# Kernel tuning notes

Hardware: AMD Instinct MI355X
Metric: run time of the kernel (lower is better)

## Reference

```python
import jax, jax.numpy as jnp
import numpy as np

C_CLIP = 10.0  # Bello et al. logit clipping constant (init arg C)


def setup_inputs() -> dict:
    key = jax.random.key(0)
    k1, k2, k3, k4, k5 = jax.random.split(key, 5)
    B, S, D = 64, 2048, 512
    scale = 1.0 / np.sqrt(D)  # ~torch Linear default init scale
    src = jax.random.normal(k1, (B, S, D), dtype=jnp.float32)
    tgt = jax.random.normal(k2, (B, 1, D), dtype=jnp.float32)
    W_q = jax.random.normal(k3, (D, D), dtype=jnp.float32) * scale
    W_ref = jax.random.normal(k4, (D, D), dtype=jnp.float32) * scale
    v = jax.random.uniform(k5, (D,), dtype=jnp.float32)  # uniform_(0, 1) as in source
    return {"src": src, "tgt": tgt, "W_q": W_q, "W_ref": W_ref, "v": v}


def reference(src, tgt, W_q, W_ref, v):
    # h = tanh(W_q(tgt) + W_ref(src))  -> [B, S, D] (tgt broadcasts over S)
    h = jnp.tanh(tgt @ W_q.T + src @ W_ref.T)
    # u = bmm(v, h^T) -> [B, 1, S]
    u = jnp.einsum("bsd,d->bs", h, v)[:, None, :]
    # logit clipping: C * tanh(u)
    logit = C_CLIP * jnp.tanh(u)
    probs = jax.nn.softmax(logit, axis=-1)  # [B, 1, S]
    # d_prime = bmm(probs, src) -> [B, 1, D]  ('Sup' path glimpse)
    d_prime = jnp.einsum("bqs,bsd->bqd", probs, src)
    return (d_prime, probs, logit)
```

## Files before the change

kernel.cpp:

```cpp
#include <hip/hip_runtime.h>
#include <math.h>

#define NB 64
#define NS 2048
#define ND 512
#define MTOT (NB * NS)
#define CCLIP 10.0f

typedef _Float16 f16x8 __attribute__((ext_vector_type(8)));
typedef _Float16 f16x4 __attribute__((ext_vector_type(4)));
typedef float f32x4 __attribute__((ext_vector_type(4)));

__device__ __forceinline__ void gl2lds16(const void* g, void* l) {
  __builtin_amdgcn_global_load_lds(
      (const __attribute__((address_space(1))) void*)(uintptr_t)g,
      (__attribute__((address_space(3))) void*)(uintptr_t)l, 16, 0, 0);
}

__device__ __forceinline__ float tanh_fast(float x) {
  float e = __expf(2.f * x);
  return 1.f - 2.f * __builtin_amdgcn_rcpf(e + 1.f);
}

__global__ __launch_bounds__(256) void cvtw_kernel(
    const float4* __restrict__ w4, _Float16* __restrict__ WhA) {
  const int idx = blockIdx.x * 256 + threadIdx.x;
  const int d = idx >> 7;
  const int k = (idx & 127) << 2;
  float4 x = w4[idx];
  f16x4 o;
  o[0] = (_Float16)x.x; o[1] = (_Float16)x.y;
  o[2] = (_Float16)x.z; o[3] = (_Float16)x.w;
  const int kt = k >> 5;
  const int kg = (k >> 3) & 3;
  const int h = k & 7;
  *(f16x4*)(WhA + ((size_t)((kt * 4 + kg) * 512 + d) * 8 + h)) = o;
}

__global__ __launch_bounds__(256) void qk_kernel(const float* __restrict__ tgt,
                                                 const float* __restrict__ Wq,
                                                 float* __restrict__ q_ws) {
  const int b = blockIdx.x >> 1;
  const int d = ((blockIdx.x & 1) << 8) + threadIdx.x;
  __shared__ float tl[ND];
  tl[threadIdx.x] = tgt[b * ND + threadIdx.x];
  tl[threadIdx.x + 256] = tgt[b * ND + threadIdx.x + 256];
  __syncthreads();
  const float4* wr = (const float4*)(Wq + (size_t)d * ND);
  float acc = 0.f;
#pragma unroll 8
  for (int k4 = 0; k4 < ND / 4; ++k4) {
    float4 w4 = wr[k4];
    acc += w4.x * tl[4 * k4 + 0] + w4.y * tl[4 * k4 + 1] +
           w4.z * tl[4 * k4 + 2] + w4.w * tl[4 * k4 + 3];
  }
  q_ws[b * ND + d] = acc;
}

__global__ __launch_bounds__(256, 2) void gemm_kernel(
    const float* __restrict__ src, const _Float16* __restrict__ WhA,
    const float* __restrict__ q_ws, const float* __restrict__ v,
    float* __restrict__ out_logit, float* __restrict__ out_probs_w,
    float* __restrict__ dp_ws) {
  __shared__ __align__(16) _Float16 sA[2][4 * 64 * 8];
  __shared__ __align__(16) _Float16 sB[2][4 * 512 * 8];
  __shared__ float ured[4 * 64];
  __shared__ float wsh[64];

  const int tid = threadIdx.x;
  const int lane = tid & 63;
  const int w = tid >> 6;
  const int s0 = blockIdx.x << 6;
  const int bb = blockIdx.x >> 5;

  const int quad = lane >> 4;
  const int l15 = lane & 15;

  const int ar = tid >> 2;
  const int akg = tid & 3;
  const float4* ap =
      (const float4*)(src + ((size_t)(s0 + ar) << 9)) + akg * 2;
  const int aoff = (akg * 64 + ar) * 8;

  const char* gB = (const char*)WhA;

  f32x4 acc[4][8];
#pragma unroll
  for (int i = 0; i < 4; ++i)
#pragma unroll
    for (int j = 0; j < 8; ++j) acc[i][j] = (f32x4){0.f, 0.f, 0.f, 0.f};

#pragma unroll
  for (int i = 0; i < 8; ++i) {
    const int c = w * 8 + i;
    gl2lds16(gB + c * 1024 + lane * 16, (char*)&sB[0][0] + c * 1024);
  }
  {
    float4 x0 = ap[0];
    float4 x1 = ap[1];
    f16x8 h;
    h[0] = (_Float16)x0.x; h[1] = (_Float16)x0.y;
    h[2] = (_Float16)x0.z; h[3] = (_Float16)x0.w;
    h[4] = (_Float16)x1.x; h[5] = (_Float16)x1.y;
    h[6] = (_Float16)x1.z; h[7] = (_Float16)x1.w;
    *(f16x8*)(&sA[0][0] + aoff) = h;
  }
  __syncthreads();

  int buf = 0;
  for (int kt = 0; kt < 16; ++kt) {
    const int nb = buf ^ 1;
    float4 x0, x1;
    if (kt < 15) {
#pragma unroll
      for (int i = 0; i < 8; ++i) {
        const int c = w * 8 + i;
        gl2lds16(gB + (size_t)(kt + 1) * 32768 + c * 1024 + lane * 16,
                 (char*)&sB[nb][0] + c * 1024);
      }
      x0 = ap[(kt + 1) * 8];
      x1 = ap[(kt + 1) * 8 + 1];
    }
    f16x8 af[4], bf[8];
#pragma unroll
    for (int i = 0; i < 4; ++i)
      af[i] = *(const f16x8*)(&sA[buf][0] + (quad * 64 + 16 * i + l15) * 8);
#pragma unroll
    for (int j = 0; j < 8; ++j)
      bf[j] = *(const f16x8*)(&sB[buf][0] +
                              (quad * 512 + w * 128 + 16 * j + l15) * 8);
#pragma unroll
    for (int i = 0; i < 4; ++i)
#pragma unroll
      for (int j = 0; j < 8; ++j)
        acc[i][j] = __builtin_amdgcn_mfma_f32_16x16x32_f16(af[i], bf[j],
                                                           acc[i][j], 0, 0, 0);
    if (kt < 15) {
      f16x8 h;
      h[0] = (_Float16)x0.x; h[1] = (_Float16)x0.y;
      h[2] = (_Float16)x0.z; h[3] = (_Float16)x0.w;
      h[4] = (_Float16)x1.x; h[5] = (_Float16)x1.y;
      h[6] = (_Float16)x1.z; h[7] = (_Float16)x1.w;
      *(f16x8*)(&sA[nb][0] + aoff) = h;
    }
    __syncthreads();
    buf = nb;
  }

  float pu[4][4];
#pragma unroll
  for (int i = 0; i < 4; ++i)
#pragma unroll
    for (int r = 0; r < 4; ++r) pu[i][r] = 0.f;

#pragma unroll
  for (int j = 0; j < 8; ++j) {
    const int dl = w * 128 + 16 * j + l15;
    const float qq = q_ws[bb * ND + dl];
    const float vv = v[dl];
#pragma unroll
    for (int i = 0; i < 4; ++i) {
      f32x4 a = acc[i][j];
#pragma unroll
      for (int r = 0; r < 4; ++r) pu[i][r] += tanh_fast(a[r] + qq) * vv;
    }
  }

#pragma unroll
  for (int i = 0; i < 4; ++i)
#pragma unroll
    for (int r = 0; r < 4; ++r) {
      float x = pu[i][r];
      x += __shfl_xor(x, 1, 16);
      x += __shfl_xor(x, 2, 16);
      x += __shfl_xor(x, 4, 16);
      x += __shfl_xor(x, 8, 16);
      pu[i][r] = x;
    }

  if (l15 == 0) {
#pragma unroll
    for (int i = 0; i < 4; ++i)
#pragma unroll
      for (int r = 0; r < 4; ++r)
        ured[w * 64 + 16 * i + quad * 4 + r] = pu[i][r];
  }
  __syncthreads();
  if (tid < 64) {
    const float u =
        ured[tid] + ured[64 + tid] + ured[128 + tid] + ured[192 + tid];
    const float lg = CCLIP * tanhf(u);
    out_logit[s0 + tid] = lg;
    const float wexp = expf(lg - CCLIP);
    out_probs_w[s0 + tid] = wexp;
    wsh[tid] = wexp;
  }
  __syncthreads();

  const int c4 = tid & 127;
  const int half = tid >> 7;
  const float4* sp = (const float4*)(src + ((size_t)s0 << 9)) + c4;
  float dx = 0.f, dy = 0.f, dz = 0.f, dw = 0.f;
  const int r0 = half << 5;
#pragma unroll 4
  for (int r = r0; r < r0 + 32; ++r) {
    const float wr = wsh[r];
    const float4 x = sp[(size_t)r * 128];
    dx += wr * x.x; dy += wr * x.y; dz += wr * x.z; dw += wr * x.w;
  }
  float4* red4 = (float4*)&sA[0][0];
  if (half) {
    float4 o; o.x = dx; o.y = dy; o.z = dz; o.w = dw;
    red4[c4] = o;
  }
  __syncthreads();
  if (!half) {
    float4 o = red4[c4];
    o.x += dx; o.y += dy; o.z += dz; o.w += dw;
    *(float4*)(dp_ws + (size_t)blockIdx.x * ND + (c4 << 2)) = o;
  }
}

__global__ __launch_bounds__(256) void fin_kernel(
    const float* __restrict__ dp_ws, float* __restrict__ out_dp,
    float* __restrict__ out_probs) {
  const int b = blockIdx.x;
  const int tid = threadIdx.x;
  __shared__ float red[4];
  __shared__ float s_inv;

  float x = 0.f;
  for (int idx = tid; idx < NS; idx += 256) x += out_probs[b * NS + idx];
#pragma unroll
  for (int m = 32; m; m >>= 1) x += __shfl_xor(x, m, 64);
  if ((tid & 63) == 0) red[tid >> 6] = x;
  __syncthreads();
  if (tid == 0) s_inv = 1.f / (red[0] + red[1] + red[2] + red[3]);
  __syncthreads();
  const float inv = s_inv;

  for (int idx = tid; idx < NS; idx += 256)
    out_probs[b * NS + idx] *= inv;

  for (int d = tid; d < ND; d += 256) {
    float acc = 0.f;
#pragma unroll 8
    for (int ch = 0; ch < 32; ++ch)
      acc += dp_ws[(size_t)(b * 32 + ch) * ND + d];
    out_dp[b * ND + d] = acc * inv;
  }
}

extern "C" void kernel_launch(void* const* d_in, const int* in_sizes, int n_in,
                              void* d_out, int out_size, void* d_ws,
                              size_t ws_size, hipStream_t stream) {
  const float* src = (const float*)d_in[0];
  const float* tgt = (const float*)d_in[1];
  const float* Wq = (const float*)d_in[2];
  const float* Wref = (const float*)d_in[3];
  const float* v = (const float*)d_in[4];

  float* out = (float*)d_out;
  float* out_dp = out;
  float* out_probs = out + NB * ND;
  float* out_logit = out + NB * ND + NB * NS;

  char* ws = (char*)d_ws;
  _Float16* WhA = (_Float16*)ws;
  float* q_ws = (float*)(ws + 524288);
  float* dp_ws = (float*)(ws + 655360);

  cvtw_kernel<<<256, 256, 0, stream>>>((const float4*)Wref, WhA);
  qk_kernel<<<2 * NB, 256, 0, stream>>>(tgt, Wq, q_ws);
  gemm_kernel<<<MTOT / 64, 256, 0, stream>>>(src, WhA, q_ws, v, out_logit,
                                             out_probs, dp_ws);
  fin_kernel<<<NB, 256, 0, stream>>>(dp_ws, out_dp, out_probs);
}
```

Baseline: 447.9 us.

## Use 128-row tiles with 8 waves, triple-buffered weight tiles and swizzled A LDS

The GEMM block doubles to 128 rows of src and 512 threads. Each group of 4 waves shares one fully loaded weight K-tile, which halves how many times the fp16 weights are fetched per row. The weight tile moves to a 3-stage LDS ring with a prefetch distance of two and explicit vmcnt waits in place of __syncthreads. The A tile uses an XOR-swizzled layout to reduce LDS bank conflicts. In exchange it uses more LDS per block (about 112KB), which may limit residency to one block per CU, and the partial-sum reduction for d_prime widens to four parts.

Result: no change. 441.4 us (-1.4%).

```diff
diff --git a/kernel.cpp b/kernel.cpp
--- a/kernel.cpp
+++ b/kernel.cpp
@@ -57,21 +57,23 @@
   q_ws[b * ND + d] = acc;
 }
 
-__global__ __launch_bounds__(256, 2) void gemm_kernel(
+__global__ __launch_bounds__(512, 2) void gemm_kernel(
     const float* __restrict__ src, const _Float16* __restrict__ WhA,
     const float* __restrict__ q_ws, const float* __restrict__ v,
     float* __restrict__ out_logit, float* __restrict__ out_probs_w,
     float* __restrict__ dp_ws) {
-  __shared__ __align__(16) _Float16 sA[2][4 * 64 * 8];
-  __shared__ __align__(16) _Float16 sB[2][4 * 512 * 8];
-  __shared__ float ured[4 * 64];
-  __shared__ float wsh[64];
+  __shared__ __align__(16) _Float16 sBall[3 * 16384];
+  __shared__ __align__(16) _Float16 sAall[2 * 4096];
+  __shared__ float ured[4 * 128];
+  __shared__ float wsh[128];
 
   const int tid = threadIdx.x;
   const int lane = tid & 63;
   const int w = tid >> 6;
-  const int s0 = blockIdx.x << 6;
-  const int bb = blockIdx.x >> 5;
+  const int h = w >> 2;
+  const int cq = w & 3;
+  const int s0 = blockIdx.x << 7;
+  const int bb = blockIdx.x >> 4;
 
   const int quad = lane >> 4;
   const int l15 = lane & 15;
@@ -80,7 +82,7 @@
   const int akg = tid & 3;
   const float4* ap =
       (const float4*)(src + ((size_t)(s0 + ar) << 9)) + akg * 2;
-  const int aoff = (akg * 64 + ar) * 8;
+  const int aoff = akg * 1024 + ((ar ^ (akg << 2)) << 3);
 
   const char* gB = (const char*)WhA;
 
@@ -90,61 +92,86 @@
 #pragma unroll
     for (int j = 0; j < 8; ++j) acc[i][j] = (f32x4){0.f, 0.f, 0.f, 0.f};
 
-#pragma unroll
-  for (int i = 0; i < 8; ++i) {
-    const int c = w * 8 + i;
-    gl2lds16(gB + c * 1024 + lane * 16, (char*)&sB[0][0] + c * 1024);
-  }
+  float4 x0 = ap[0];
+  float4 x1 = ap[1];
   {
-    float4 x0 = ap[0];
-    float4 x1 = ap[1];
-    f16x8 h;
-    h[0] = (_Float16)x0.x; h[1] = (_Float16)x0.y;
-    h[2] = (_Float16)x0.z; h[3] = (_Float16)x0.w;
-    h[4] = (_Float16)x1.x; h[5] = (_Float16)x1.y;
-    h[6] = (_Float16)x1.z; h[7] = (_Float16)x1.w;
-    *(f16x8*)(&sA[0][0] + aoff) = h;
-  }
-  __syncthreads();
-
-  int buf = 0;
+    f16x8 hh;
+    hh[0] = (_Float16)x0.x; hh[1] = (_Float16)x0.y;
+    hh[2] = (_Float16)x0.z; hh[3] = (_Float16)x0.w;
+    hh[4] = (_Float16)x1.x; hh[5] = (_Float16)x1.y;
+    hh[6] = (_Float16)x1.z; hh[7] = (_Float16)x1.w;
+    *(f16x8*)(sAall + aoff) = hh;
+  }
+#pragma unroll
+  for (int i = 0; i < 4; ++i) {
+    const int c = w * 4 + i;
+    gl2lds16(gB + c * 1024 + lane * 16, (char*)sBall + c * 1024);
+  }
+  x0 = ap[8];
+  x1 = ap[9];
+#pragma unroll
+  for (int i = 0; i < 4; ++i) {
+    const int c = w * 4 + i;
+    gl2lds16(gB + 32768 + c * 1024 + lane * 16,
+             (char*)(sBall + 16384) + c * 1024);
+  }
+  __builtin_amdgcn_sched_barrier(0);
+  asm volatile("s_waitcnt vmcnt(0)" ::: "memory");
+  asm volatile("s_waitcnt lgkmcnt(0)" ::: "memory");
+  __builtin_amdgcn_s_barrier();
+  __builtin_amdgcn_sched_barrier(0);
+
   for (int kt = 0; kt < 16; ++kt) {
-    const int nb = buf ^ 1;
-    float4 x0, x1;
+    const _Float16* sB = sBall + (kt % 3) * 16384;
+    const _Float16* sA = sAall + (kt & 1) * 4096;
+
+    f16x8 af[4], bf[8];
+#pragma unroll
+    for (int i = 0; i < 4; ++i) {
+      const int row = h * 64 + 16 * i + l15;
+      af[i] = *(const f16x8*)(sA + quad * 1024 + ((row ^ (quad << 2)) << 3));
+    }
+#pragma unroll
+    for (int j = 0; j < 8; ++j)
+      bf[j] = *(const f16x8*)(sB +
+                              ((quad * 512 + cq * 128 + 16 * j + l15) << 3));
+
     if (kt < 15) {
-#pragma unroll
-      for (int i = 0; i < 8; ++i) {
-        const int c = w * 8 + i;
-        gl2lds16(gB + (size_t)(kt + 1) * 32768 + c * 1024 + lane * 16,
-                 (char*)&sB[nb][0] + c * 1024);
+      f16x8 hh;
+      hh[0] = (_Float16)x0.x; hh[1] = (_Float16)x0.y;
+      hh[2] = (_Float16)x0.z; hh[3] = (_Float16)x0.w;
+      hh[4] = (_Float16)x1.x; hh[5] = (_Float16)x1.y;
+      hh[6] = (_Float16)x1.z; hh[7] = (_Float16)x1.w;
+      *(f16x8*)(sAall + ((kt + 1) & 1) * 4096 + aoff) = hh;
+    }
+    if (kt < 14) {
+      x0 = ap[(kt + 2) * 8];
+      x1 = ap[(kt + 2) * 8 + 1];
+      char* sBn = (char*)(sBall + ((kt + 2) % 3) * 16384);
+#pragma unroll
+      for (int i = 0; i < 4; ++i) {
+        const int c = w * 4 + i;
+        gl2lds16(gB + (size_t)(kt + 2) * 32768 + c * 1024 + lane * 16,
+                 sBn + c * 1024);
       }
-      x0 = ap[(kt + 1) * 8];
-      x1 = ap[(kt + 1) * 8 + 1];
-    }
-    f16x8 af[4], bf[8];
-#pragma unroll
-    for (int i = 0; i < 4; ++i)
-      af[i] = *(const f16x8*)(&sA[buf][0] + (quad * 64 + 16 * i + l15) * 8);
-#pragma unroll
-    for (int j = 0; j < 8; ++j)
-      bf[j] = *(const f16x8*)(&sB[buf][0] +
-                              (quad * 512 + w * 128 + 16 * j + l15) * 8);
+    }
+
 #pragma unroll
     for (int i = 0; i < 4; ++i)
 #pragma unroll
       for (int j = 0; j < 8; ++j)
         acc[i][j] = __builtin_amdgcn_mfma_f32_16x16x32_f16(af[i], bf[j],
                                                            acc[i][j], 0, 0, 0);
-    if (kt < 15) {
-      f16x8 h;
-      h[0] = (_Float16)x0.x; h[1] = (_Float16)x0.y;
-      h[2] = (_Float16)x0.z; h[3] = (_Float16)x0.w;
-      h[4] = (_Float16)x1.x; h[5] = (_Float16)x1.y;
-      h[6] = (_Float16)x1.z; h[7] = (_Float16)x1.w;
-      *(f16x8*)(&sA[nb][0] + aoff) = h;
-    }
-    __syncthreads();
-    buf = nb;
+
+    __builtin_amdgcn_sched_barrier(0);
+    if (kt < 14) {
+      asm volatile("s_waitcnt vmcnt(6)" ::: "memory");
+    } else {
+      asm volatile("s_waitcnt vmcnt(0)" ::: "memory");
+    }
+    asm volatile("s_waitcnt lgkmcnt(0)" ::: "memory");
+    __builtin_amdgcn_s_barrier();
+    __builtin_amdgcn_sched_barrier(0);
   }
 
   float pu[4][4];
@@ -155,7 +182,7 @@
 
 #pragma unroll
   for (int j = 0; j < 8; ++j) {
-    const int dl = w * 128 + 16 * j + l15;
+    const int dl = cq * 128 + 16 * j + l15;
     const float qq = q_ws[bb * ND + dl];
     const float vv = v[dl];
 #pragma unroll
@@ -183,12 +210,12 @@
     for (int i = 0; i < 4; ++i)
 #pragma unroll
       for (int r = 0; r < 4; ++r)
-        ured[w * 64 + 16 * i + quad * 4 + r] = pu[i][r];
-  }
-  __syncthreads();
-  if (tid < 64) {
+        ured[cq * 128 + h * 64 + 16 * i + quad * 4 + r] = pu[i][r];
+  }
+  __syncthreads();
+  if (tid < 128) {
     const float u =
-        ured[tid] + ured[64 + tid] + ured[128 + tid] + ured[192 + tid];
+        ured[tid] + ured[128 + tid] + ured[256 + tid] + ured[384 + tid];
     const float lg = CCLIP * tanhf(u);
     out_logit[s0 + tid] = lg;
     const float wexp = expf(lg - CCLIP);
@@ -198,25 +225,32 @@
   __syncthreads();
 
   const int c4 = tid & 127;
-  const int half = tid >> 7;
+  const int part = tid >> 7;
   const float4* sp = (const float4*)(src + ((size_t)s0 << 9)) + c4;
   float dx = 0.f, dy = 0.f, dz = 0.f, dw = 0.f;
-  const int r0 = half << 5;
+  const int r0 = part << 5;
 #pragma unroll 4
   for (int r = r0; r < r0 + 32; ++r) {
     const float wr = wsh[r];
     const float4 x = sp[(size_t)r * 128];
     dx += wr * x.x; dy += wr * x.y; dz += wr * x.z; dw += wr * x.w;
   }
-  float4* red4 = (float4*)&sA[0][0];
-  if (half) {
+  float4* red4 = (float4*)sBall;
+  {
     float4 o; o.x = dx; o.y = dy; o.z = dz; o.w = dw;
-    red4[c4] = o;
-  }
-  __syncthreads();
-  if (!half) {
-    float4 o = red4[c4];
-    o.x += dx; o.y += dy; o.z += dz; o.w += dw;
+    red4[part * 128 + c4] = o;
+  }
+  __syncthreads();
+  if (tid < 128) {
+    float4 a0 = red4[c4];
+    float4 a1 = red4[128 + c4];
+    float4 a2 = red4[256 + c4];
+    float4 a3 = red4[384 + c4];
+    float4 o;
+    o.x = a0.x + a1.x + a2.x + a3.x;
+    o.y = a0.y + a1.y + a2.y + a3.y;
+    o.z = a0.z + a1.z + a2.z + a3.z;
+    o.w = a0.w + a1.w + a2.w + a3.w;
     *(float4*)(dp_ws + (size_t)blockIdx.x * ND + (c4 << 2)) = o;
   }
 }
@@ -244,9 +278,9 @@
 
   for (int d = tid; d < ND; d += 256) {
     float acc = 0.f;
-#pragma unroll 8
-    for (int ch = 0; ch < 32; ++ch)
-      acc += dp_ws[(size_t)(b * 32 + ch) * ND + d];
+#pragma unroll
+    for (int ch = 0; ch < 16; ++ch)
+      acc += dp_ws[(size_t)(b * 16 + ch) * ND + d];
     out_dp[b * ND + d] = acc * inv;
   }
 }
@@ -272,7 +306,7 @@
 
   cvtw_kernel<<<256, 256, 0, stream>>>((const float4*)Wref, WhA);
   qk_kernel<<<2 * NB, 256, 0, stream>>>(tgt, Wq, q_ws);
-  gemm_kernel<<<MTOT / 64, 256, 0, stream>>>(src, WhA, q_ws, v, out_logit,
-                                             out_probs, dp_ws);
+  gemm_kernel<<<MTOT / 128, 512, 0, stream>>>(src, WhA, q_ws, v, out_logit,
+                                              out_probs, dp_ws);
   fin_kernel<<<NB, 256, 0, stream>>>(dp_ws, out_dp, out_probs);
 }
```

## Load W_ref fragments directly from global into registers instead of LDS staging

Applied to the files above, without the earlier changes.

Converts W_ref into a pre-swizzled fp16 layout in which each lane's MFMA B-fragment is a contiguous 16-byte load, so the GEMM reads B straight from global/L2 into registers. This drops the large sB LDS double buffer and the global-to-LDS copies. It also XOR-swizzles the sA layout to avoid LDS bank conflicts and issues the next A tile's load and store before the MFMAs. The smaller LDS footprint could allow more resident blocks, but every block now re-reads W_ref from cache each k-step with less latency hiding, since the B loads are not prefetched.

Measured after the change: 453.9 us. Within noise of the previous version (+1.3%).

```diff
diff --git a/kernel.cpp b/kernel.cpp
--- a/kernel.cpp
+++ b/kernel.cpp
@@ -11,30 +11,29 @@
 typedef _Float16 f16x4 __attribute__((ext_vector_type(4)));
 typedef float f32x4 __attribute__((ext_vector_type(4)));
 
-__device__ __forceinline__ void gl2lds16(const void* g, void* l) {
-  __builtin_amdgcn_global_load_lds(
-      (const __attribute__((address_space(1))) void*)(uintptr_t)g,
-      (__attribute__((address_space(3))) void*)(uintptr_t)l, 16, 0, 0);
-}
-
 __device__ __forceinline__ float tanh_fast(float x) {
   float e = __expf(2.f * x);
   return 1.f - 2.f * __builtin_amdgcn_rcpf(e + 1.f);
 }
 
-__global__ __launch_bounds__(256) void cvtw_kernel(
-    const float4* __restrict__ w4, _Float16* __restrict__ WhA) {
-  const int idx = blockIdx.x * 256 + threadIdx.x;
-  const int d = idx >> 7;
-  const int k = (idx & 127) << 2;
-  float4 x = w4[idx];
-  f16x4 o;
-  o[0] = (_Float16)x.x; o[1] = (_Float16)x.y;
-  o[2] = (_Float16)x.z; o[3] = (_Float16)x.w;
-  const int kt = k >> 5;
-  const int kg = (k >> 3) & 3;
-  const int h = k & 7;
-  *(f16x4*)(WhA + ((size_t)((kt * 4 + kg) * 512 + d) * 8 + h)) = o;
+__global__ __launch_bounds__(256) void cvtw2_kernel(
+    const float* __restrict__ Wref, _Float16* __restrict__ Wc) {
+  const int g = blockIdx.x * 256 + threadIdx.x;
+  const int lane = g & 63;
+  const int rest = g >> 6;
+  const int c32 = rest & 31;
+  const int kt = rest >> 5;
+  const int col = c32 * 16 + (lane & 15);
+  const int k = kt * 32 + ((lane >> 4) & 3) * 8;
+  const float4* in = (const float4*)(Wref + (size_t)col * ND + k);
+  float4 a = in[0];
+  float4 b = in[1];
+  f16x8 o;
+  o[0] = (_Float16)a.x; o[1] = (_Float16)a.y;
+  o[2] = (_Float16)a.z; o[3] = (_Float16)a.w;
+  o[4] = (_Float16)b.x; o[5] = (_Float16)b.y;
+  o[6] = (_Float16)b.z; o[7] = (_Float16)b.w;
+  *(f16x8*)(Wc + (size_t)g * 8) = o;
 }
 
 __global__ __launch_bounds__(256) void qk_kernel(const float* __restrict__ tgt,
@@ -58,18 +57,18 @@
 }
 
 __global__ __launch_bounds__(256, 2) void gemm_kernel(
-    const float* __restrict__ src, const _Float16* __restrict__ WhA,
+    const float* __restrict__ src, const _Float16* __restrict__ Wc,
     const float* __restrict__ q_ws, const float* __restrict__ v,
     float* __restrict__ out_logit, float* __restrict__ out_probs_w,
     float* __restrict__ dp_ws) {
-  __shared__ __align__(16) _Float16 sA[2][4 * 64 * 8];
-  __shared__ __align__(16) _Float16 sB[2][4 * 512 * 8];
+  __shared__ __align__(16) _Float16 sAall[2 * 4 * 64 * 8];
   __shared__ float ured[4 * 64];
   __shared__ float wsh[64];
 
   const int tid = threadIdx.x;
   const int lane = tid & 63;
   const int w = tid >> 6;
+  const int cq = w;
   const int s0 = blockIdx.x << 6;
   const int bb = blockIdx.x >> 5;
 
@@ -80,9 +79,9 @@
   const int akg = tid & 3;
   const float4* ap =
       (const float4*)(src + ((size_t)(s0 + ar) << 9)) + akg * 2;
-  const int aoff = (akg * 64 + ar) * 8;
-
-  const char* gB = (const char*)WhA;
+  const int aoff = akg * 512 + ((ar ^ (akg << 2)) << 3);
+
+  const _Float16* wb = Wc + ((size_t)(cq * 8) * 64 + lane) * 8;
 
   f32x4 acc[4][8];
 #pragma unroll
@@ -90,61 +89,53 @@
 #pragma unroll
     for (int j = 0; j < 8; ++j) acc[i][j] = (f32x4){0.f, 0.f, 0.f, 0.f};
 
-#pragma unroll
-  for (int i = 0; i < 8; ++i) {
-    const int c = w * 8 + i;
-    gl2lds16(gB + c * 1024 + lane * 16, (char*)&sB[0][0] + c * 1024);
-  }
   {
     float4 x0 = ap[0];
     float4 x1 = ap[1];
-    f16x8 h;
-    h[0] = (_Float16)x0.x; h[1] = (_Float16)x0.y;
-    h[2] = (_Float16)x0.z; h[3] = (_Float16)x0.w;
-    h[4] = (_Float16)x1.x; h[5] = (_Float16)x1.y;
-    h[6] = (_Float16)x1.z; h[7] = (_Float16)x1.w;
-    *(f16x8*)(&sA[0][0] + aoff) = h;
-  }
-  __syncthreads();
-
-  int buf = 0;
+    f16x8 hh;
+    hh[0] = (_Float16)x0.x; hh[1] = (_Float16)x0.y;
+    hh[2] = (_Float16)x0.z; hh[3] = (_Float16)x0.w;
+    hh[4] = (_Float16)x1.x; hh[5] = (_Float16)x1.y;
+    hh[6] = (_Float16)x1.z; hh[7] = (_Float16)x1.w;
+    *(f16x8*)(sAall + aoff) = hh;
+  }
+  __syncthreads();
+
   for (int kt = 0; kt < 16; ++kt) {
-    const int nb = buf ^ 1;
-    float4 x0, x1;
+    const _Float16* sA = sAall + (kt & 1) * 2048;
+
+    f16x8 bf[8];
+    const _Float16* wk = wb + (size_t)(kt * 32) * 512;
+#pragma unroll
+    for (int j = 0; j < 8; ++j)
+      bf[j] = *(const f16x8*)(wk + (size_t)j * 512);
+
+    f16x8 af[4];
+#pragma unroll
+    for (int i = 0; i < 4; ++i) {
+      const int row = 16 * i + l15;
+      af[i] = *(const f16x8*)(sA + quad * 512 + ((row ^ (quad << 2)) << 3));
+    }
+
     if (kt < 15) {
-#pragma unroll
-      for (int i = 0; i < 8; ++i) {
-        const int c = w * 8 + i;
-        gl2lds16(gB + (size_t)(kt + 1) * 32768 + c * 1024 + lane * 16,
-                 (char*)&sB[nb][0] + c * 1024);
-      }
-      x0 = ap[(kt + 1) * 8];
-      x1 = ap[(kt + 1) * 8 + 1];
-    }
-    f16x8 af[4], bf[8];
-#pragma unroll
-    for (int i = 0; i < 4; ++i)
-      af[i] = *(const f16x8*)(&sA[buf][0] + (quad * 64 + 16 * i + l15) * 8);
-#pragma unroll
-    for (int j = 0; j < 8; ++j)
-      bf[j] = *(const f16x8*)(&sB[buf][0] +
-                              (quad * 512 + w * 128 + 16 * j + l15) * 8);
+      float4 x0 = ap[(kt + 1) * 8];
+      float4 x1 = ap[(kt + 1) * 8 + 1];
+      f16x8 hh;
+      hh[0] = (_Float16)x0.x; hh[1] = (_Float16)x0.y;
+      hh[2] = (_Float16)x0.z; hh[3] = (_Float16)x0.w;
+      hh[4] = (_Float16)x1.x; hh[5] = (_Float16)x1.y;
+      hh[6] = (_Float16)x1.z; hh[7] = (_Float16)x1.w;
+      *(f16x8*)(sAall + ((kt + 1) & 1) * 2048 + aoff) = hh;
+    }
+
 #pragma unroll
     for (int i = 0; i < 4; ++i)
 #pragma unroll
       for (int j = 0; j < 8; ++j)
         acc[i][j] = __builtin_amdgcn_mfma_f32_16x16x32_f16(af[i], bf[j],
                                                            acc[i][j], 0, 0, 0);
-    if (kt < 15) {
-      f16x8 h;
-      h[0] = (_Float16)x0.x; h[1] = (_Float16)x0.y;
-      h[2] = (_Float16)x0.z; h[3] = (_Float16)x0.w;
-      h[4] = (_Float16)x1.x; h[5] = (_Float16)x1.y;
-      h[6] = (_Float16)x1.z; h[7] = (_Float16)x1.w;
-      *(f16x8*)(&sA[nb][0] + aoff) = h;
-    }
+
     __syncthreads();
-    buf = nb;
   }
 
   float pu[4][4];
@@ -155,7 +146,7 @@
 
 #pragma unroll
   for (int j = 0; j < 8; ++j) {
-    const int dl = w * 128 + 16 * j + l15;
+    const int dl = cq * 128 + 16 * j + l15;
     const float qq = q_ws[bb * ND + dl];
     const float vv = v[dl];
 #pragma unroll
@@ -208,7 +199,7 @@
     const float4 x = sp[(size_t)r * 128];
     dx += wr * x.x; dy += wr * x.y; dz += wr * x.z; dw += wr * x.w;
   }
-  float4* red4 = (float4*)&sA[0][0];
+  float4* red4 = (float4*)sAall;
   if (half) {
     float4 o; o.x = dx; o.y = dy; o.z = dz; o.w = dw;
     red4[c4] = o;
@@ -266,13 +257,13 @@
   float* out_logit = out + NB * ND + NB * NS;
 
   char* ws = (char*)d_ws;
-  _Float16* WhA = (_Float16*)ws;
+  _Float16* Wc = (_Float16*)ws;
   float* q_ws = (float*)(ws + 524288);
   float* dp_ws = (float*)(ws + 655360);
 
-  cvtw_kernel<<<256, 256, 0, stream>>>((const float4*)Wref, WhA);
+  cvtw2_kernel<<<128, 256, 0, stream>>>(Wref, Wc);
   qk_kernel<<<2 * NB, 256, 0, stream>>>(tgt, Wq, q_ws);
-  gemm_kernel<<<MTOT / 64, 256, 0, stream>>>(src, WhA, q_ws, v, out_logit,
+  gemm_kernel<<<MTOT / 64, 256, 0, stream>>>(src, Wc, q_ws, v, out_logit,
                                              out_probs, dp_ws);
   fin_kernel<<<NB, 256, 0, stream>>>(dp_ws, out_dp, out_probs);
 }
```
